# Kernel tuning notes

Measured on AMD Instinct MI355X. Metric: run time of the kernel, lower is better.

Reference implementation:

```python
import jax, jax.numpy as jnp
import numpy as np

N_NODES = 100000
N_EDGES = 1000000
HID = 128


def _lin(x, W, b):
    # torch nn.Linear: x @ W.T + b
    return x @ W.T + b


def _comp_agg(n_feat, e_vec, s, d, n_nodes):
    """u_sub_e message + sum aggregation + in-degree^-0.5 normalization."""
    msg = n_feat[s] - e_vec[None, :]                     # [E, D]
    agg = jax.ops.segment_sum(msg, d, num_segments=n_nodes)  # [N, D]
    deg = jax.ops.segment_sum(jnp.ones_like(d, dtype=n_feat.dtype), d,
                              num_segments=n_nodes)      # in-degrees
    norm = jnp.maximum(deg, 1.0) ** -0.5
    return agg * norm[:, None]


def setup_inputs() -> dict:
    key = jax.random.key(0)
    ks = jax.random.split(key, 16)
    sc = 1.0 / np.sqrt(HID)
    return {
        "n_feat": jax.random.normal(ks[0], (N_NODES, HID), jnp.float32),
        "e_feat_fwd": jax.random.normal(ks[1], (HID,), jnp.float32),
        "e_feat_rev": jax.random.normal(ks[2], (HID,), jnp.float32),
        "W_I": jax.random.normal(ks[3], (HID, HID), jnp.float32) * sc,
        "b_I": jax.random.normal(ks[4], (HID,), jnp.float32) * sc,
        "W_O": jax.random.normal(ks[5], (HID, HID), jnp.float32) * sc,
        "b_O": jax.random.normal(ks[6], (HID,), jnp.float32) * sc,
        "W_S": jax.random.normal(ks[7], (HID, HID), jnp.float32) * sc,
        "b_S": jax.random.normal(ks[8], (HID,), jnp.float32) * sc,
        "W_rel": jax.random.normal(ks[9], (HID, HID), jnp.float32) * sc,
        "b_rel": jax.random.normal(ks[10], (HID,), jnp.float32) * sc,
        "src": jax.random.randint(ks[11], (N_EDGES,), 0, N_NODES, jnp.int32),
        "dst": jax.random.randint(ks[12], (N_EDGES,), 0, N_NODES, jnp.int32),
    }


def reference(n_feat, e_feat_fwd, e_feat_rev, W_I, b_I, W_O, b_O,
              W_S, b_S, W_rel, b_rel, src, dst):
    n_nodes = n_feat.shape[0]
    # forward relation: edges src->dst, composed with e_feat_fwd, then W_I
    comp_f = _comp_agg(n_feat, e_feat_fwd, src, dst, n_nodes)
    h_f = _lin(comp_f, W_I, b_I)
    # reverse relation ('_inv'): edges dst->src, composed with e_feat_rev, then W_O
    comp_r = _comp_agg(n_feat, e_feat_rev, dst, src, n_nodes)
    h_r = _lin(comp_r, W_O, b_O)
    # self-loop path
    h_s = _lin(n_feat, W_S, b_S)
    # mix: dropout is identity at p=0.0; activation is None
    n_out = (h_f + h_r) * (2.0 / 3.0) + h_s * (1.0 / 3.0)
    # edge feature update (formula 2)
    e_out_fwd = _lin(e_feat_fwd, W_rel, b_rel)
    e_out_rev = _lin(e_feat_rev, W_rel, b_rel)
    return (n_out, e_out_fwd, e_out_rev)
```

## Files before the change

kernel.cpp:

```cpp
#include <hip/hip_runtime.h>
#include <stdint.h>

#define NN 100000
#define NE 1000000
#define HID 128
#define NB 391

typedef __attribute__((ext_vector_type(4))) float f32x4;
typedef __attribute__((ext_vector_type(4))) unsigned u32x4;
typedef __attribute__((ext_vector_type(8))) short short8;
typedef __attribute__((ext_vector_type(8))) __bf16 bf16x8;

union V8 { short8 s; bf16x8 b; };
union AW { unsigned w[4]; bf16x8 b; };
union BP { struct { unsigned long long lo, hi; } u; short8 s; bf16x8 b; };

__device__ __forceinline__ unsigned short f2bf(float f) {
    unsigned u = __float_as_uint(f);
    unsigned r = u + 0x7fffu + ((u >> 16) & 1u);
    return (unsigned short)(r >> 16);
}

__global__ __launch_bounds__(256) void k_prep(
        const float* __restrict__ n_feat, unsigned* __restrict__ nfbf_u,
        const float* __restrict__ WI, const float* __restrict__ WO,
        const float* __restrict__ WS, const float* __restrict__ bI,
        const float* __restrict__ bO, const float* __restrict__ bS,
        unsigned short* __restrict__ Wbf, float* __restrict__ biasc,
        const float* __restrict__ W_rel, const float* __restrict__ b_rel,
        const float* __restrict__ e_fwd, const float* __restrict__ e_rev,
        const int* __restrict__ src, const int* __restrict__ dst,
        int* __restrict__ bcntD, int* __restrict__ bcntS,
        float* __restrict__ outp) {
    __shared__ int hD[NB], hS[NB];
    int bb = blockIdx.x;
    int tid = threadIdx.x;
    const int NC = NN * HID / 8 / 256;

    if (bb < NC) {
        int t = bb * 256 + tid;
        const f32x4* pin = (const f32x4*)n_feat;
        f32x4 a = pin[2 * t], b = pin[2 * t + 1];
        u32x4 o;
        o[0] = (unsigned)f2bf(a[0]) | ((unsigned)f2bf(a[1]) << 16);
        o[1] = (unsigned)f2bf(a[2]) | ((unsigned)f2bf(a[3]) << 16);
        o[2] = (unsigned)f2bf(b[0]) | ((unsigned)f2bf(b[1]) << 16);
        o[3] = (unsigned)f2bf(b[2]) | ((unsigned)f2bf(b[3]) << 16);
        ((u32x4*)nfbf_u)[t] = o;
    } else if (bb < NC + 192) {
        int t = (bb - NC) * 256 + tid;
        int p = t >> 14, i = t & 16383;
        const float* Wsrc = (p == 0) ? WI : ((p == 1) ? WO : WS);
        float scale = (p == 2) ? (1.0f / 3.0f) : (2.0f / 3.0f);
        Wbf[t] = f2bf(Wsrc[i] * scale);
        if (t < HID) biasc[t] = (2.0f / 3.0f) * (bI[t] + bO[t]) + (1.0f / 3.0f) * bS[t];
    } else if (bb == NC + 192) {
        int cc = tid & 127;
        const float* e = (tid < 128) ? e_fwd : e_rev;
        float s = b_rel[cc];
        #pragma unroll 4
        for (int k = 0; k < HID; ++k) s += W_rel[cc * HID + k] * e[k];
        outp[(size_t)NN * HID + ((tid < 128) ? 0 : HID) + cc] = s;
    } else if (bb == NC + 193) {
        if (tid < 64) nfbf_u[(size_t)NN * 64 + tid] = 0;
    } else {
        for (int b = tid; b < NB; b += 256) { hD[b] = 0; hS[b] = 0; }
        __syncthreads();
        int base = (bb - NC - 194) * 8192;
        #pragma unroll
        for (int i = 0; i < 32; ++i) {
            int e = base + i * 256 + tid;
            if (e < NE) {
                atomicAdd(&hD[dst[e] >> 8], 1);
                atomicAdd(&hS[src[e] >> 8], 1);
            }
        }
        __syncthreads();
        for (int b = tid; b < NB; b += 256) {
            if (hD[b]) atomicAdd(&bcntD[b], hD[b]);
            if (hS[b]) atomicAdd(&bcntS[b], hS[b]);
        }
    }
}

__global__ __launch_bounds__(512) void k_bucketscan(
        const int* __restrict__ bcntD, const int* __restrict__ bcntS,
        int* __restrict__ bbaseD, int* __restrict__ bbaseS,
        int* __restrict__ bcurD, int* __restrict__ bcurS) {
    __shared__ int wtot[8];
    int t = threadIdx.x, lane = t & 63, w = t >> 6;
    #pragma unroll
    for (int dir = 0; dir < 2; ++dir) {
        const int* cnt = dir ? bcntS : bcntD;
        int* bb = dir ? bbaseS : bbaseD;
        int* bc = dir ? bcurS : bcurD;
        int v = (t < NB) ? cnt[t] : 0;
        int x = v;
        #pragma unroll
        for (int off = 1; off < 64; off <<= 1) {
            int y = __shfl_up(x, off);
            if (lane >= off) x += y;
        }
        if (lane == 63) wtot[w] = x;
        __syncthreads();
        int wbase = 0;
        for (int j = 0; j < w; ++j) wbase += wtot[j];
        int incl = wbase + x;
        if (t < NB) { bb[t] = incl - v; bc[t] = incl - v; }
        if (t == NB - 1) bb[NB] = incl;
        __syncthreads();
    }
}

__global__ __launch_bounds__(256) void k_binfill(
        const int* __restrict__ src, const int* __restrict__ dst,
        int* __restrict__ bcurD, int* __restrict__ bcurS,
        unsigned* __restrict__ binD, unsigned* __restrict__ binS) {
    __shared__ int hD[NB], hS[NB];
    int tid = threadIdx.x;
    for (int b = tid; b < NB; b += 256) { hD[b] = 0; hS[b] = 0; }
    __syncthreads();
    int base = blockIdx.x * 8192;
    int s[32], d[32];
    #pragma unroll
    for (int i = 0; i < 32; ++i) {
        int e = base + i * 256 + tid;
        s[i] = -1; d[i] = -1;
        if (e < NE) { s[i] = src[e]; d[i] = dst[e]; }
    }
    #pragma unroll
    for (int i = 0; i < 32; ++i) {
        if (s[i] >= 0) {
            atomicAdd(&hD[d[i] >> 8], 1);
            atomicAdd(&hS[s[i] >> 8], 1);
        }
    }
    __syncthreads();
    for (int b = tid; b < NB; b += 256) {
        int c = hD[b];
        hD[b] = c ? atomicAdd(&bcurD[b], c) : 0;
        c = hS[b];
        hS[b] = c ? atomicAdd(&bcurS[b], c) : 0;
    }
    __syncthreads();
    #pragma unroll
    for (int i = 0; i < 32; ++i) {
        if (s[i] >= 0) {
            int p = atomicAdd(&hD[d[i] >> 8], 1);
            binD[p] = ((unsigned)s[i] << 8) | ((unsigned)d[i] & 255u);
            int q = atomicAdd(&hS[s[i] >> 8], 1);
            binS[q] = ((unsigned)d[i] << 8) | ((unsigned)s[i] & 255u);
        }
    }
}

__global__ __launch_bounds__(256) void k_bucketsort(
        const unsigned* __restrict__ binD, const unsigned* __restrict__ binS,
        const int* __restrict__ bbaseD, const int* __restrict__ bbaseS,
        int* __restrict__ row_in, int* __restrict__ row_out,
        unsigned* __restrict__ col2_in, unsigned* __restrict__ col2_out) {
    __shared__ int c[256];
    __shared__ int wtot[4];
    int bid = blockIdx.x;
    int dir = (bid >= NB) ? 1 : 0;
    int b = dir ? (bid - NB) : bid;
    const unsigned* bin = dir ? binS : binD;
    const int* bb = dir ? bbaseS : bbaseD;
    int* row = dir ? row_out : row_in;
    unsigned* col2 = dir ? col2_out : col2_in;

    int tid = threadIdx.x, lane = tid & 63, w = tid >> 6;
    int base = bb[b], cnt = bb[b + 1] - base;
    int node0 = b << 8;
    int M = NN - node0; if (M > 256) M = 256;

    c[tid] = 0;
    __syncthreads();
    for (int k = tid; k < cnt; k += 256)
        atomicAdd(&c[bin[base + k] & 255u], 1);
    __syncthreads();
    int v = c[tid];
    int x = v;
    #pragma unroll
    for (int off = 1; off < 64; off <<= 1) {
        int y = __shfl_up(x, off);
        if (lane >= off) x += y;
    }
    if (lane == 63) wtot[w] = x;
    __syncthreads();
    int wbase = 0;
    for (int j = 0; j < w; ++j) wbase += wtot[j];
    int incl = wbase + x;
    if (tid < M) row[node0 + tid + 1] = base + incl;
    if (b == 0 && tid == 0) row[0] = 0;
    __syncthreads();
    c[tid] = base + incl - v;
    __syncthreads();
    for (int k = tid; k < cnt; k += 256) {
        unsigned pk = bin[base + k];
        int p = atomicAdd(&c[pk & 255u], 1);
        col2[p] = ((pk >> 8) << 4) | (pk & 15u);
    }
}

typedef __attribute__((address_space(3))) unsigned char as3u8;
typedef __attribute__((address_space(3))) unsigned as3u32;
typedef __attribute__((address_space(1))) const unsigned as1cu32;

__global__ __launch_bounds__(256) void k_agg(
        const unsigned char* __restrict__ nf,
        const float* __restrict__ e_fwd, const float* __restrict__ e_rev,
        const int* __restrict__ row_in, const unsigned* __restrict__ col2_in,
        const int* __restrict__ row_out, const unsigned* __restrict__ col2_out,
        const unsigned short* __restrict__ Wbf, const float* __restrict__ biasc,
        float* __restrict__ outp) {
    __shared__ __align__(1024) unsigned char smem[4][4096];
    int warp = threadIdx.x >> 6;
    int l = threadIdx.x & 63;
    int gbase = blockIdx.x * 2;
    int dir = warp & 1;
    int grp = gbase + (warp >> 1);
    int node0 = grp << 4;

    const int* row = dir ? row_out : row_in;
    const unsigned* col2 = dir ? col2_out : col2_in;
    const float* ev = dir ? e_rev : e_fwd;

    int lm = l & 15;
    int q = l >> 4;
    int kg = q * 8;
    int la = l & 15;
    int kslot = (l & 31) >> 1;

    as3u8* ldsp = (as3u8*)&smem[warp][0];
    as3u8* trp  = ldsp + (((q & 1) << 8) + (lm << 3));

    int ecur = row[node0];
    int eend = row[node0 + 16];

    f32x4 acc[8];
    #pragma unroll
    for (int nb = 0; nb < 8; ++nb) {
        acc[nb][0] = 0.0f; acc[nb][1] = 0.0f; acc[nb][2] = 0.0f; acc[nb][3] = 0.0f;
    }

    unsigned pk = (ecur + la < eend) ? col2[ecur + la] : ((unsigned)NN << 4);
    while (ecur < eend) {
        int enext = ecur + 16;
        int rowk = __shfl((int)(pk >> 4), kslot);
        const unsigned char* gp = nf + (((size_t)rowk) << 8) +
                                  ((l >> 5) << 5) + ((l & 1) << 4);
#define GLL(I) __builtin_amdgcn_global_load_lds( \
            (as1cu32*)(gp + (I) * 64), \
            (as3u32*)(ldsp + (I) * 1024), 16, 0, 0)
        GLL(0); GLL(1); GLL(2); GLL(3);
#undef GLL
        unsigned pknext = (enext < eend)
            ? ((enext + la < eend) ? col2[enext + la] : ((unsigned)NN << 4))
            : 0u;

        int dl = (int)(pk & 15u);
        AW a;
        #pragma unroll
        for (int j2 = 0; j2 < 4; ++j2) {
            int d0 = __shfl(dl, kg + 2 * j2);
            int d1 = __shfl(dl, kg + 2 * j2 + 1);
            unsigned lo = (q < 2 && d0 == lm) ? 0x3F80u : 0u;
            unsigned hi = (q < 2 && d1 == lm) ? 0x3F80u : 0u;
            a.w[j2] = lo | (hi << 16);
        }

        asm volatile("s_waitcnt vmcnt(0)" ::: "memory");
        __builtin_amdgcn_sched_barrier(0);

        unsigned long long t0[8], t1[8];
        #pragma unroll
        for (int nb = 0; nb < 8; ++nb) {
            asm volatile("ds_read_b64_tr_b16 %0, %1 offset:%2"
                         : "=&v"(t0[nb]) : "v"(trp), "i"(nb * 512));
            asm volatile("ds_read_b64_tr_b16 %0, %1 offset:%2"
                         : "=&v"(t1[nb]) : "v"(trp), "i"(nb * 512 + 128));
        }
        asm volatile("s_waitcnt lgkmcnt(0)" ::: "memory");
        __builtin_amdgcn_sched_barrier(0);

        #pragma unroll
        for (int nb = 0; nb < 8; ++nb) {
            BP bp;
            bp.u.lo = t0[nb];
            bp.u.hi = t1[nb];
            acc[nb] = __builtin_amdgcn_mfma_f32_16x16x32_bf16(a.b, bp.b, acc[nb], 0, 0, 0);
        }
        pk = pknext;
        ecur = enext;
    }

    int rp = row[node0 + ((l < 17) ? l : 16)];
    int degi = __shfl(rp, l + 1) - rp;
    float degfv = (float)degi;
    float rnv = (degi > 0) ? (1.0f / sqrtf(degfv)) : 1.0f;

    float evv[8];
    #pragma unroll
    for (int nb = 0; nb < 8; ++nb) evv[nb] = ev[nb * 16 + lm];

    #pragma unroll
    for (int ip = 0; ip < 2; ++ip) {
        int m0 = q * 4 + 2 * ip;
        float dm0 = __shfl(degfv, m0), rm0 = __shfl(rnv, m0);
        float dm1 = __shfl(degfv, m0 + 1), rm1 = __shfl(rnv, m0 + 1);
        #pragma unroll
        for (int nb = 0; nb < 8; ++nb) {
            float v0 = (acc[nb][2 * ip]     - dm0 * evv[nb]) * rm0;
            float v1 = (acc[nb][2 * ip + 1] - dm1 * evv[nb]) * rm1;
            unsigned dw = (unsigned)f2bf(v0) | ((unsigned)f2bf(v1) << 16);
            *(as3u32*)(ldsp + (nb * 16 + lm) * 32 + q * 8 + ip * 4) = dw;
        }
    }
    __syncthreads();

    const unsigned short* nfu = (const unsigned short*)nf;
    int obase = warp * 2;
    f32x4 D[2][2];
    #pragma unroll
    for (int a2 = 0; a2 < 2; ++a2)
        #pragma unroll
        for (int b2 = 0; b2 < 2; ++b2) {
            D[a2][b2][0] = 0.0f; D[a2][b2][1] = 0.0f;
            D[a2][b2][2] = 0.0f; D[a2][b2][3] = 0.0f;
        }

    #pragma unroll
    for (int p = 0; p < 3; ++p) {
        V8 A[2][4];
        #pragma unroll
        for (int ob2 = 0; ob2 < 2; ++ob2)
            #pragma unroll
            for (int kb = 0; kb < 4; ++kb)
                A[ob2][kb].s = *(const short8*)(Wbf + p * 16384 +
                    ((obase + ob2) * 16 + lm) * 128 + kb * 32 + q * 8);
        #pragma unroll
        for (int gg = 0; gg < 2; ++gg) {
            BP B[4];
            if (p < 2) {
                unsigned long long tb0[4], tb1[4];
                as3u8* ib = (as3u8*)&smem[gg * 2 + p][0] + ((lm << 3) + (q << 8));
                #pragma unroll
                for (int kb = 0; kb < 4; ++kb) {
                    asm volatile("ds_read_b64_tr_b16 %0, %1 offset:%2"
                                 : "=&v"(tb0[kb]) : "v"(ib), "i"(kb * 1024));
                    asm volatile("ds_read_b64_tr_b16 %0, %1 offset:%2"
                                 : "=&v"(tb1[kb]) : "v"(ib), "i"(kb * 1024 + 128));
                }
                asm volatile("s_waitcnt lgkmcnt(0)" ::: "memory");
                __builtin_amdgcn_sched_barrier(0);
                #pragma unroll
                for (int kb = 0; kb < 4; ++kb) { B[kb].u.lo = tb0[kb]; B[kb].u.hi = tb1[kb]; }
            } else {
                int node = (gbase + gg) * 16 + lm;
                #pragma unroll
                for (int kb = 0; kb < 4; ++kb)
                    B[kb].s = *(const short8*)(nfu + (size_t)node * 128 + kb * 32 + q * 8);
            }
            #pragma unroll
            for (int ob2 = 0; ob2 < 2; ++ob2)
                #pragma unroll
                for (int kb = 0; kb < 4; ++kb)
                    D[ob2][gg] = __builtin_amdgcn_mfma_f32_16x16x32_bf16(
                        A[ob2][kb].b, B[kb].b, D[ob2][gg], 0, 0, 0);
        }
    }

    #pragma unroll
    for (int ob2 = 0; ob2 < 2; ++ob2) {
        int o0 = (obase + ob2) * 16 + q * 4;
        f32x4 bias = *(const f32x4*)(biasc + o0);
        #pragma unroll
        for (int gg = 0; gg < 2; ++gg) {
            int node = (gbase + gg) * 16 + lm;
            f32x4 r = D[ob2][gg] + bias;
            *(f32x4*)(outp + (size_t)node * 128 + o0) = r;
        }
    }
}

extern "C" void kernel_launch(void* const* d_in, const int* in_sizes, int n_in,
                              void* d_out, int out_size, void* d_ws, size_t ws_size,
                              hipStream_t stream) {
    const float* n_feat = (const float*)d_in[0];
    const float* e_fwd  = (const float*)d_in[1];
    const float* e_rev  = (const float*)d_in[2];
    const float* W_I    = (const float*)d_in[3];
    const float* b_I    = (const float*)d_in[4];
    const float* W_O    = (const float*)d_in[5];
    const float* b_O    = (const float*)d_in[6];
    const float* W_S    = (const float*)d_in[7];
    const float* b_S    = (const float*)d_in[8];
    const float* W_rel  = (const float*)d_in[9];
    const float* b_rel  = (const float*)d_in[10];
    const int*   src    = (const int*)d_in[11];
    const int*   dst    = (const int*)d_in[12];
    float* outp = (float*)d_out;

    uint8_t* ws = (uint8_t*)d_ws;
    size_t off = 0;
    auto alloc = [&](size_t bytes) -> size_t {
        size_t r = off;
        off = (off + bytes + 255) & ~(size_t)255;
        return r;
    };
    size_t o_nfbf   = alloc((size_t)(NN + 1) * HID * 2);
    size_t o_wbf    = alloc((size_t)3 * HID * HID * 2);
    size_t o_biasc  = alloc(HID * 4);
    size_t o_rowin  = alloc((size_t)(NN + 1) * 4);
    size_t o_rowout = alloc((size_t)(NN + 1) * 4);
    size_t o_col2in = alloc((size_t)NE * 4);
    size_t o_col2out= alloc((size_t)NE * 4);
    size_t o_binD   = alloc((size_t)NE * 4);
    size_t o_binS   = alloc((size_t)NE * 4);
    size_t o_bcnt   = alloc((size_t)2 * NB * 4);
    size_t o_bbaseD = alloc((size_t)(NB + 1) * 4);
    size_t o_bbaseS = alloc((size_t)(NB + 1) * 4);
    size_t o_bcurD  = alloc((size_t)NB * 4);
    size_t o_bcurS  = alloc((size_t)NB * 4);
    (void)ws_size; (void)in_sizes; (void)n_in; (void)out_size;

    unsigned short* nfbf  = (unsigned short*)(ws + o_nfbf);
    unsigned short* wbf   = (unsigned short*)(ws + o_wbf);
    float*     biasc      = (float*)(ws + o_biasc);
    int* row_in  = (int*)(ws + o_rowin);
    int* row_out = (int*)(ws + o_rowout);
    unsigned* col2_in  = (unsigned*)(ws + o_col2in);
    unsigned* col2_out = (unsigned*)(ws + o_col2out);
    unsigned* binD = (unsigned*)(ws + o_binD);
    unsigned* binS = (unsigned*)(ws + o_binS);
    int* bcntD   = (int*)(ws + o_bcnt);
    int* bcntS   = bcntD + NB;
    int* bbaseD  = (int*)(ws + o_bbaseD);
    int* bbaseS  = (int*)(ws + o_bbaseS);
    int* bcurD   = (int*)(ws + o_bcurD);
    int* bcurS   = (int*)(ws + o_bcurS);

    (void)hipMemsetAsync(ws + o_bcnt, 0, (size_t)2 * NB * 4, stream);

    k_prep<<<6567, 256, 0, stream>>>(n_feat, (unsigned*)nfbf,
                                     W_I, W_O, W_S, b_I, b_O, b_S, wbf, biasc,
                                     W_rel, b_rel, e_fwd, e_rev,
                                     src, dst, bcntD, bcntS, outp);

    k_bucketscan<<<1, 512, 0, stream>>>(bcntD, bcntS, bbaseD, bbaseS, bcurD, bcurS);
    k_binfill<<<(NE + 8191) / 8192, 256, 0, stream>>>(src, dst, bcurD, bcurS, binD, binS);
    k_bucketsort<<<2 * NB, 256, 0, stream>>>(binD, binS, bbaseD, bbaseS,
                                             row_in, row_out, col2_in, col2_out);

    k_agg<<<3125, 256, 0, stream>>>((const unsigned char*)nfbf, e_fwd, e_rev,
                                    row_in, col2_in, row_out, col2_out,
                                    wbf, biasc, outp);
}
```

Baseline: 189.4 us.

## Double-buffer LDS gather in aggregation loop to overlap loads with MFMA

Each wave's LDS staging area grows from 4 KB to 8 KB, so the next 16-edge chunk of neighbor rows is issued with global_load_lds into the alternate buffer before the current chunk is transposed and fed to MFMA. Index prefetch is also moved two chunks ahead. The goal is to hide the gather latency that the old loop exposed by waiting on vmcnt(0) every iteration. In exchange it doubles LDS per block, which may limit occupancy, and it relies on the vmcnt(5) count staying correct for the in-flight loads.

Result: slower. 194.9 us (+2.9%).

```diff
diff --git a/kernel.cpp b/kernel.cpp
--- a/kernel.cpp
+++ b/kernel.cpp
@@ -214,7 +214,7 @@
         const int* __restrict__ row_out, const unsigned* __restrict__ col2_out,
         const unsigned short* __restrict__ Wbf, const float* __restrict__ biasc,
         float* __restrict__ outp) {
-    __shared__ __align__(1024) unsigned char smem[4][4096];
+    __shared__ __align__(1024) unsigned char smem[4][8192];
     int warp = threadIdx.x >> 6;
     int l = threadIdx.x & 63;
     int gbase = blockIdx.x * 2;
@@ -229,11 +229,11 @@
     int lm = l & 15;
     int q = l >> 4;
     int kg = q * 8;
-    int la = l & 15;
     int kslot = (l & 31) >> 1;
 
     as3u8* ldsp = (as3u8*)&smem[warp][0];
     as3u8* trp  = ldsp + (((q & 1) << 8) + (lm << 3));
+    const unsigned SENT = ((unsigned)NN << 4);
 
     int ecur = row[node0];
     int eend = row[node0 + 16];
@@ -244,56 +244,74 @@
         acc[nb][0] = 0.0f; acc[nb][1] = 0.0f; acc[nb][2] = 0.0f; acc[nb][3] = 0.0f;
     }
 
-    unsigned pk = (ecur + la < eend) ? col2[ecur + la] : ((unsigned)NN << 4);
-    while (ecur < eend) {
-        int enext = ecur + 16;
-        int rowk = __shfl((int)(pk >> 4), kslot);
-        const unsigned char* gp = nf + (((size_t)rowk) << 8) +
-                                  ((l >> 5) << 5) + ((l & 1) << 4);
-#define GLL(I) __builtin_amdgcn_global_load_lds( \
-            (as1cu32*)(gp + (I) * 64), \
-            (as3u32*)(ldsp + (I) * 1024), 16, 0, 0)
-        GLL(0); GLL(1); GLL(2); GLL(3);
-#undef GLL
-        unsigned pknext = (enext < eend)
-            ? ((enext + la < eend) ? col2[enext + la] : ((unsigned)NN << 4))
-            : 0u;
-
-        int dl = (int)(pk & 15u);
-        AW a;
-        #pragma unroll
-        for (int j2 = 0; j2 < 4; ++j2) {
-            int d0 = __shfl(dl, kg + 2 * j2);
-            int d1 = __shfl(dl, kg + 2 * j2 + 1);
-            unsigned lo = (q < 2 && d0 == lm) ? 0x3F80u : 0u;
-            unsigned hi = (q < 2 && d1 == lm) ? 0x3F80u : 0u;
-            a.w[j2] = lo | (hi << 16);
-        }
-
-        asm volatile("s_waitcnt vmcnt(0)" ::: "memory");
-        __builtin_amdgcn_sched_barrier(0);
-
-        unsigned long long t0[8], t1[8];
-        #pragma unroll
-        for (int nb = 0; nb < 8; ++nb) {
-            asm volatile("ds_read_b64_tr_b16 %0, %1 offset:%2"
-                         : "=&v"(t0[nb]) : "v"(trp), "i"(nb * 512));
-            asm volatile("ds_read_b64_tr_b16 %0, %1 offset:%2"
-                         : "=&v"(t1[nb]) : "v"(trp), "i"(nb * 512 + 128));
-        }
-        asm volatile("s_waitcnt lgkmcnt(0)" ::: "memory");
-        __builtin_amdgcn_sched_barrier(0);
-
-        #pragma unroll
-        for (int nb = 0; nb < 8; ++nb) {
-            BP bp;
-            bp.u.lo = t0[nb];
-            bp.u.hi = t1[nb];
-            acc[nb] = __builtin_amdgcn_mfma_f32_16x16x32_bf16(a.b, bp.b, acc[nb], 0, 0, 0);
-        }
-        pk = pknext;
-        ecur = enext;
-    }
+#define STAGE(BUFOFF, PK) do { \
+        int rowk_ = __shfl((int)((PK) >> 4), kslot); \
+        const unsigned char* gp_ = nf + (((size_t)rowk_) << 8) + \
+                                   ((l >> 5) << 5) + ((l & 1) << 4); \
+        __builtin_amdgcn_global_load_lds((as1cu32*)(gp_ + 0),   (as3u32*)(ldsp + (BUFOFF) + 0),    16, 0, 0); \
+        __builtin_amdgcn_global_load_lds((as1cu32*)(gp_ + 64),  (as3u32*)(ldsp + (BUFOFF) + 1024), 16, 0, 0); \
+        __builtin_amdgcn_global_load_lds((as1cu32*)(gp_ + 128), (as3u32*)(ldsp + (BUFOFF) + 2048), 16, 0, 0); \
+        __builtin_amdgcn_global_load_lds((as1cu32*)(gp_ + 192), (as3u32*)(ldsp + (BUFOFF) + 3072), 16, 0, 0); \
+    } while (0)
+
+#define COMPUTE(BUFOFF, AFRAG) do { \
+        unsigned long long t0_[8], t1_[8]; \
+        _Pragma("unroll") \
+        for (int nb = 0; nb < 8; ++nb) { \
+            asm volatile("ds_read_b64_tr_b16 %0, %1 offset:%2" \
+                         : "=&v"(t0_[nb]) : "v"(trp + (BUFOFF)), "i"(nb * 512)); \
+            asm volatile("ds_read_b64_tr_b16 %0, %1 offset:%2" \
+                         : "=&v"(t1_[nb]) : "v"(trp + (BUFOFF)), "i"(nb * 512 + 128)); \
+        } \
+        asm volatile("s_waitcnt lgkmcnt(0)" ::: "memory"); \
+        __builtin_amdgcn_sched_barrier(0); \
+        _Pragma("unroll") \
+        for (int nb = 0; nb < 8; ++nb) { \
+            BP bp_; \
+            bp_.u.lo = t0_[nb]; \
+            bp_.u.hi = t1_[nb]; \
+            acc[nb] = __builtin_amdgcn_mfma_f32_16x16x32_bf16((AFRAG).b, bp_.b, acc[nb], 0, 0, 0); \
+        } \
+    } while (0)
+
+    if (ecur < eend) {
+        unsigned pkA = (ecur + lm < eend) ? col2[ecur + lm] : SENT;
+        unsigned pkB = SENT;
+        if (ecur + 16 < eend)
+            pkB = (ecur + 16 + lm < eend) ? col2[ecur + 16 + lm] : SENT;
+        STAGE(0, pkA);
+        int bp = 0;
+        while (true) {
+            int enext = ecur + 16;
+            int dl = (int)(pkA & 15u);
+            AW a;
+            #pragma unroll
+            for (int j2 = 0; j2 < 4; ++j2) {
+                int d0 = __shfl(dl, kg + 2 * j2);
+                int d1 = __shfl(dl, kg + 2 * j2 + 1);
+                unsigned lo = (q < 2 && d0 == lm) ? 0x3F80u : 0u;
+                unsigned hi = (q < 2 && d1 == lm) ? 0x3F80u : 0u;
+                a.w[j2] = lo | (hi << 16);
+            }
+            if (enext < eend) {
+                unsigned pkC = SENT;
+                if (enext + 16 < eend)
+                    pkC = (enext + 16 + lm < eend) ? col2[enext + 16 + lm] : SENT;
+                STAGE((bp ^ 1) * 4096, pkB);
+                asm volatile("s_waitcnt vmcnt(5)" ::: "memory");
+                __builtin_amdgcn_sched_barrier(0);
+                COMPUTE(bp * 4096, a);
+                pkA = pkB; pkB = pkC; bp ^= 1; ecur = enext;
+            } else {
+                asm volatile("s_waitcnt vmcnt(0)" ::: "memory");
+                __builtin_amdgcn_sched_barrier(0);
+                COMPUTE(bp * 4096, a);
+                break;
+            }
+        }
+    }
+#undef STAGE
+#undef COMPUTE
 
     int rp = row[node0 + ((l < 17) ? l : 16)];
     int degi = __shfl(rp, l + 1) - rp;
```
